# Kernel tuning notes

Hardware: AMD Instinct MI355X
Metric: run time of the kernel (lower is better)

The kernel has to match this reference:

```python
import jax, jax.numpy as jnp
import numpy as np


def setup_inputs() -> dict:
    key = jax.random.key(0)
    kq, kk, kv = jax.random.split(key, 3)
    shape = (2, 16, 2048, 64)  # [B, H, S, D]
    return {
        "q": jax.random.normal(kq, shape, dtype=jnp.float32),
        "k": jax.random.normal(kk, shape, dtype=jnp.float32),
        "v": jax.random.normal(kv, shape, dtype=jnp.float32),
    }


def reference(q, k, v):
    # scores = q @ k^T / sqrt(d_k)  -> [B, H, S, S]
    d_k = k.shape[-1]
    scale = 1.0 / jnp.sqrt(jnp.asarray(d_k, dtype=q.dtype))
    scores = jnp.einsum("bhqd,bhkd->bhqk", q, k) * scale
    seq_len = q.shape[-2]
    # causal mask: position q attends to k <= q
    causal = jnp.tril(jnp.ones((seq_len, seq_len), dtype=bool))
    scores = jnp.where(causal, scores, jnp.asarray(-jnp.inf, dtype=scores.dtype))
    probs = jax.nn.softmax(scores, axis=-1)
    return jnp.einsum("bhqk,bhkd->bhqd", probs, v)
```

## Files before the change

### kernel.cpp

```cpp
#include <hip/hip_runtime.h>
#include <hip/hip_bf16.h>

typedef short bf16x8 __attribute__((ext_vector_type(8)));
typedef short bf16x4 __attribute__((ext_vector_type(4)));
typedef float f32x4  __attribute__((ext_vector_type(4)));
typedef float f32x16 __attribute__((ext_vector_type(16)));

#define D_DIM 64
#define SEQ 2048
#define BHD (SEQ * D_DIM)
#define SCALE_L2E 0.1803368801111204f

__device__ __forceinline__ unsigned short f2bf(float f) {
    unsigned u = __builtin_bit_cast(unsigned, f);
    u += 0x7fffu + ((u >> 16) & 1u);
    return (unsigned short)(u >> 16);
}

__device__ __forceinline__ unsigned swz(unsigned row, unsigned colByte) {
    return (row * 128u + colByte) ^ ((row & 7u) << 4);
}

__device__ __forceinline__ void gl_lds(const unsigned short* g, unsigned char* lds_generic,
                                       unsigned lds_off) {
    __builtin_amdgcn_global_load_lds(
        (const __attribute__((address_space(1))) void*)g,
        (__attribute__((address_space(3))) void*)(lds_generic + lds_off), 16, 0, 0);
}

__device__ __forceinline__ float fexp2(float x) {
    float r; asm("v_exp_f32 %0, %1" : "=v"(r) : "v"(x)); return r;
}
__device__ __forceinline__ unsigned cvtpk(float lo, float hi) {
    unsigned r; asm("v_cvt_pk_bf16_f32 %0, %1, %2" : "=v"(r) : "v"(lo), "v"(hi)); return r;
}

__global__ __launch_bounds__(256) void prep_kernel(const float* __restrict__ K,
                                                   const float* __restrict__ V,
                                                   unsigned short* __restrict__ Kb,
                                                   unsigned short* __restrict__ Vt) {
    __shared__ unsigned short t[64][66];
    const int st = blockIdx.x;
    const int bh = blockIdx.y;
    const int tid = threadIdx.x;
    const size_t base = (size_t)bh * BHD;

    const float* ksrc = K + base + st * 4096;
    unsigned short* kdst = Kb + base + st * 4096;
    #pragma unroll
    for (int j = 0; j < 2; ++j) {
        int e = (j * 256 + tid) * 8;
        float4 a = *(const float4*)(ksrc + e);
        float4 b = *(const float4*)(ksrc + e + 4);
        bf16x8 o;
        o[0] = (short)f2bf(a.x); o[1] = (short)f2bf(a.y);
        o[2] = (short)f2bf(a.z); o[3] = (short)f2bf(a.w);
        o[4] = (short)f2bf(b.x); o[5] = (short)f2bf(b.y);
        o[6] = (short)f2bf(b.z); o[7] = (short)f2bf(b.w);
        *(bf16x8*)(kdst + e) = o;
    }

    const float* vb = V + base + st * 64 * D_DIM;
    #pragma unroll
    for (int j = 0; j < 4; ++j) {
        int n = tid + 256 * j;
        int r = n >> 4;
        int c = (n & 15) << 2;
        float4 v = *(const float4*)(vb + r * D_DIM + c);
        t[r][c + 0] = f2bf(v.x); t[r][c + 1] = f2bf(v.y);
        t[r][c + 2] = f2bf(v.z); t[r][c + 3] = f2bf(v.w);
    }
    __syncthreads();
    #pragma unroll
    for (int j = 0; j < 2; ++j) {
        int m = tid + 256 * j;
        int d = m >> 3;
        int s8 = (m & 7) << 3;
        bf16x8 o;
        #pragma unroll
        for (int e = 0; e < 8; ++e) o[e] = (short)t[s8 + e][d];
        *(bf16x8*)(Vt + base + (size_t)d * SEQ + st * 64 + s8) = o;
    }
}

__global__ __launch_bounds__(512, 4) void attn_fwd(const float* __restrict__ Qp,
                                                   const unsigned short* __restrict__ Kb,
                                                   const unsigned short* __restrict__ Vtb,
                                                   float* __restrict__ Op) {
    __shared__ __align__(16) unsigned char lds[65536];

    int id = blockIdx.y * gridDim.x + blockIdx.x;
    int j  = id >> 3;
    const int bh = (id & 7) * 4 + (j >> 4);
    const int jq = j & 15;
    const int qtile = (j < 32) ? (15 - jq) : jq;

    const int tid  = threadIdx.x;
    const int w    = tid >> 6;
    const int lane = tid & 63;
    const int l31  = lane & 31;
    const int hi2  = lane >> 5;
    const int wsub = w & 3;
    const int par  = w >> 2;

    const int qlo = qtile * 128 + wsub * 32;
    const int t_w = qlo >> 6;
    const int qg  = qlo + l31;
    const int nt  = qtile + 1;

    const size_t base = (size_t)bh * BHD;
    const float* qp = Qp + base;
    const unsigned short* kb = Kb + base;
    const unsigned short* vt = Vtb + base;
    float* op = Op + base;

    const int srow = tid >> 3;
    const int scb  = ((tid & 7) << 4) ^ ((srow & 7) << 4);
    const int kOff = srow * D_DIM + (scb >> 1);
    const int vOff = srow * SEQ + (scb >> 1);
    const unsigned sdst = (unsigned)tid * 16u;

    auto STAGE = [&](int it) {
        unsigned bb = (unsigned)(it & 1) * 32768u;
        const unsigned short* kg = kb + (size_t)(2 * it) * 4096 + kOff;
        const unsigned short* vg = vt + (size_t)(2 * it) * 64 + vOff;
        gl_lds(kg, lds, bb + sdst);
        gl_lds(vg, lds, bb + 8192u + sdst);
        gl_lds(kg + 4096, lds, bb + 16384u + sdst);
        gl_lds(vg + 64, lds, bb + 24576u + sdst);
    };

    const float* qsrc = qp + (size_t)qg * D_DIM + hi2 * 8;
    float4 qraw[8];
    #pragma unroll
    for (int dk = 0; dk < 4; ++dk) {
        qraw[2 * dk]     = *(const float4*)(qsrc + dk * 16);
        qraw[2 * dk + 1] = *(const float4*)(qsrc + dk * 16 + 4);
    }
    STAGE(0);

    bf16x8 qB[4];
    #pragma unroll
    for (int dk = 0; dk < 4; ++dk) {
        float4 a = qraw[2 * dk], b = qraw[2 * dk + 1];
        bf16x8 v;
        v[0] = (short)f2bf(a.x * SCALE_L2E); v[1] = (short)f2bf(a.y * SCALE_L2E);
        v[2] = (short)f2bf(a.z * SCALE_L2E); v[3] = (short)f2bf(a.w * SCALE_L2E);
        v[4] = (short)f2bf(b.x * SCALE_L2E); v[5] = (short)f2bf(b.y * SCALE_L2E);
        v[6] = (short)f2bf(b.z * SCALE_L2E); v[7] = (short)f2bf(b.w * SCALE_L2E);
        qB[dk] = v;
    }

    f32x16 acc0 = {}, acc1 = {};
    float m_r = -3.0e38f, l_r = 0.f;

    #pragma unroll 1
    for (int it = 0; it < nt; ++it) {
        asm volatile("s_waitcnt vmcnt(0)" ::: "memory");
        __builtin_amdgcn_s_barrier();
        __builtin_amdgcn_sched_barrier(0);
        if (it + 1 < nt) STAGE(it + 1);

        const int tile = 2 * it + par;
        if (tile <= t_w) {
            const unsigned kbuf = (unsigned)(it & 1) * 32768u + (unsigned)par * 16384u;
            const unsigned vbuf = kbuf + 8192u;

            f32x16 st0 = {}, st1 = {};
            __builtin_amdgcn_s_setprio(1);
            #pragma unroll
            for (int dk = 0; dk < 4; ++dk) {
                bf16x8 k0 = *(const bf16x8*)&lds[kbuf +
                    swz((unsigned)l31, (unsigned)(dk * 32 + hi2 * 16))];
                bf16x8 k1 = *(const bf16x8*)&lds[kbuf +
                    swz((unsigned)(32 + l31), (unsigned)(dk * 32 + hi2 * 16))];
                st0 = __builtin_amdgcn_mfma_f32_32x32x16_bf16(k0, qB[dk], st0, 0, 0, 0);
                st1 = __builtin_amdgcn_mfma_f32_32x32x16_bf16(k1, qB[dk], st1, 0, 0, 0);
            }
            __builtin_amdgcn_s_setprio(0);

            if (tile == t_w) {
                #pragma unroll
                for (int r = 0; r < 16; ++r) {
                    int kvb = tile * 64 + (r & 3) + 8 * (r >> 2) + 4 * hi2;
                    if (kvb > qg)      st0[r] = -3.0e38f;
                    if (kvb + 32 > qg) st1[r] = -3.0e38f;
                }
            }

            float m8[8];
            #pragma unroll
            for (int r = 0; r < 8; ++r)
                m8[r] = fmaxf(fmaxf(st0[r], st0[r + 8]), fmaxf(st1[r], st1[r + 8]));
            #pragma unroll
            for (int r = 0; r < 4; ++r) m8[r] = fmaxf(m8[r], m8[r + 4]);
            float mx = fmaxf(fmaxf(m8[0], m8[1]), fmaxf(m8[2], m8[3]));
            mx = fmaxf(mx, __shfl_xor(mx, 32));

            float mn;
            if (__all(mx <= m_r + 8.0f)) {
                mn = m_r;
            } else {
                mn = fmaxf(m_r, mx);
                float sc = fexp2(m_r - mn);
                m_r = mn;
                l_r *= sc;
                #pragma unroll
                for (int r = 0; r < 16; ++r) { acc0[r] *= sc; acc1[r] *= sc; }
            }

            #pragma unroll
            for (int r = 0; r < 16; ++r) st0[r] = fexp2(st0[r] - mn);
            #pragma unroll
            for (int r = 0; r < 16; ++r) st1[r] = fexp2(st1[r] - mn);
            float s16[16];
            #pragma unroll
            for (int r = 0; r < 16; ++r) s16[r] = st0[r] + st1[r];
            #pragma unroll
            for (int r = 0; r < 8; ++r) s16[r] += s16[r + 8];
            #pragma unroll
            for (int r = 0; r < 4; ++r) s16[r] += s16[r + 4];
            float rs = (s16[0] + s16[1]) + (s16[2] + s16[3]);
            rs += __shfl_xor(rs, 32);
            l_r += rs;

            bf16x8 pf[4];
            #pragma unroll
            for (int b2 = 0; b2 < 2; ++b2) {
                unsigned W[4][2];
                #pragma unroll
                for (int c = 0; c < 4; ++c) {
                    float v0 = b2 ? st1[4 * c + 0] : st0[4 * c + 0];
                    float v1 = b2 ? st1[4 * c + 1] : st0[4 * c + 1];
                    float v2 = b2 ? st1[4 * c + 2] : st0[4 * c + 2];
                    float v3 = b2 ? st1[4 * c + 3] : st0[4 * c + 3];
                    W[c][0] = cvtpk(v0, v1);
                    W[c][1] = cvtpk(v2, v3);
                }
                #pragma unroll
                for (int m = 0; m < 2; ++m) {
                    unsigned s0 = hi2 ? W[2 * m][0] : W[2 * m + 1][0];
                    unsigned s1 = hi2 ? W[2 * m][1] : W[2 * m + 1][1];
                    unsigned r0 = (unsigned)__shfl_xor((int)s0, 32);
                    unsigned r1 = (unsigned)__shfl_xor((int)s1, 32);
                    int4 fw;
                    fw.x = (int)(hi2 ? r0 : W[2 * m][0]);
                    fw.y = (int)(hi2 ? r1 : W[2 * m][1]);
                    fw.z = (int)(hi2 ? W[2 * m + 1][0] : r0);
                    fw.w = (int)(hi2 ? W[2 * m + 1][1] : r1);
                    pf[b2 * 2 + m] = __builtin_bit_cast(bf16x8, fw);
                }
            }

            __builtin_amdgcn_s_setprio(1);
            #pragma unroll
            for (int mm = 0; mm < 4; ++mm) {
                bf16x8 va0 = *(const bf16x8*)&lds[vbuf +
                    swz((unsigned)l31, (unsigned)(mm * 32 + hi2 * 16))];
                bf16x8 va1 = *(const bf16x8*)&lds[vbuf +
                    swz((unsigned)(32 + l31), (unsigned)(mm * 32 + hi2 * 16))];
                acc0 = __builtin_amdgcn_mfma_f32_32x32x16_bf16(va0, pf[mm], acc0, 0, 0, 0);
                acc1 = __builtin_amdgcn_mfma_f32_32x32x16_bf16(va1, pf[mm], acc1, 0, 0, 0);
            }
            __builtin_amdgcn_s_setprio(0);
        }
    }

    __builtin_amdgcn_s_barrier();
    const unsigned mbase = (unsigned)wsub * (64u * 144u) + (unsigned)lane * 144u;
    if (w >= 4) {
        #pragma unroll
        for (int c = 0; c < 4; ++c) {
            f32x4 q0 = {acc0[4 * c], acc0[4 * c + 1], acc0[4 * c + 2], acc0[4 * c + 3]};
            *(f32x4*)&lds[mbase + c * 16] = q0;
            f32x4 q1 = {acc1[4 * c], acc1[4 * c + 1], acc1[4 * c + 2], acc1[4 * c + 3]};
            *(f32x4*)&lds[mbase + 64 + c * 16] = q1;
        }
        *(float*)&lds[mbase + 128] = m_r;
        *(float*)&lds[mbase + 132] = l_r;
    }
    __builtin_amdgcn_s_barrier();
    if (w < 4) {
        float m2 = *(const float*)&lds[mbase + 128];
        float l2 = *(const float*)&lds[mbase + 132];
        float m  = fmaxf(m_r, m2);
        float a1 = fexp2(m_r - m);
        float a2 = fexp2(m2 - m);
        float l  = a1 * l_r + a2 * l2;
        float inv = 1.f / l;
        #pragma unroll
        for (int c = 0; c < 4; ++c) {
            f32x4 p0 = *(const f32x4*)&lds[mbase + c * 16];
            f32x4 p1 = *(const f32x4*)&lds[mbase + 64 + c * 16];
            float4 o0, o1;
            o0.x = (a1 * acc0[4 * c + 0] + a2 * p0[0]) * inv;
            o0.y = (a1 * acc0[4 * c + 1] + a2 * p0[1]) * inv;
            o0.z = (a1 * acc0[4 * c + 2] + a2 * p0[2]) * inv;
            o0.w = (a1 * acc0[4 * c + 3] + a2 * p0[3]) * inv;
            o1.x = (a1 * acc1[4 * c + 0] + a2 * p1[0]) * inv;
            o1.y = (a1 * acc1[4 * c + 1] + a2 * p1[1]) * inv;
            o1.z = (a1 * acc1[4 * c + 2] + a2 * p1[2]) * inv;
            o1.w = (a1 * acc1[4 * c + 3] + a2 * p1[3]) * inv;
            *(float4*)(op + (size_t)qg * D_DIM + 8 * c + 4 * hi2) = o0;
            *(float4*)(op + (size_t)qg * D_DIM + 32 + 8 * c + 4 * hi2) = o1;
        }
    }
}

__global__ __launch_bounds__(256) void attn_fwd_fb(
    const float* __restrict__ Qp, const float* __restrict__ Kp,
    const float* __restrict__ Vp, float* __restrict__ Op, int S)
{
    __shared__ __align__(16) unsigned char lds_k[64 * 128];
    __shared__ __align__(16) unsigned char lds_vt[64 * 128];
    __shared__ __align__(16) unsigned char lds_p[4 * 16 * 128];

    const int qt = blockIdx.x, bh = blockIdx.y, tid = threadIdx.x;
    const int w = tid >> 6, lane = tid & 63, lo = lane & 15, hi = lane >> 4;
    const size_t base = (size_t)bh * S * D_DIM;
    const float* qp = Qp + base; const float* kp = Kp + base;
    const float* vp = Vp + base; float* op = Op + base;
    const int qw = qt * 64 + w * 16;

    auto swzl = [](unsigned row, unsigned colByte) {
        return (row * 128u + colByte) ^ ((row & 7u) << 4);
    };

    bf16x8 qf[2];
    {
        const float* src = qp + (size_t)(qw + lo) * D_DIM + hi * 8;
        #pragma unroll
        for (int f = 0; f < 2; ++f) {
            float4 a = *(const float4*)(src + f * 32);
            float4 b = *(const float4*)(src + f * 32 + 4);
            bf16x8 v;
            v[0] = (short)f2bf(a.x * 0.125f); v[1] = (short)f2bf(a.y * 0.125f);
            v[2] = (short)f2bf(a.z * 0.125f); v[3] = (short)f2bf(a.w * 0.125f);
            v[4] = (short)f2bf(b.x * 0.125f); v[5] = (short)f2bf(b.y * 0.125f);
            v[6] = (short)f2bf(b.z * 0.125f); v[7] = (short)f2bf(b.w * 0.125f);
            qf[f] = v;
        }
    }
    f32x4 o_acc[4]; float m_r[4], l_r[4];
    #pragma unroll
    for (int r = 0; r < 4; ++r) { m_r[r] = -__builtin_inff(); l_r[r] = 0.f; }
    #pragma unroll
    for (int dt = 0; dt < 4; ++dt) o_acc[dt] = (f32x4){0.f, 0.f, 0.f, 0.f};
    const unsigned pbase = (unsigned)w * 2048u;

    for (int t = 0; t <= qt; ++t) {
        const size_t kv0 = (size_t)t * 64;
        __syncthreads();
        #pragma unroll
        for (int jj = 0; jj < 4; ++jj) {
            int n = tid + 256 * jj;
            int r = n >> 4, c = (n & 15) << 2;
            float4 kk = *(const float4*)(kp + (kv0 + r) * D_DIM + c);
            bf16x4 kbv;
            kbv[0] = (short)f2bf(kk.x); kbv[1] = (short)f2bf(kk.y);
            kbv[2] = (short)f2bf(kk.z); kbv[3] = (short)f2bf(kk.w);
            *(bf16x4*)&lds_k[swzl((unsigned)r, (unsigned)c * 2)] = kbv;
            float4 vv = *(const float4*)(vp + (kv0 + r) * D_DIM + c);
            *(unsigned short*)&lds_vt[swzl((unsigned)(c + 0), (unsigned)r * 2)] = f2bf(vv.x);
            *(unsigned short*)&lds_vt[swzl((unsigned)(c + 1), (unsigned)r * 2)] = f2bf(vv.y);
            *(unsigned short*)&lds_vt[swzl((unsigned)(c + 2), (unsigned)r * 2)] = f2bf(vv.z);
            *(unsigned short*)&lds_vt[swzl((unsigned)(c + 3), (unsigned)r * 2)] = f2bf(vv.w);
        }
        __syncthreads();

        float sc[4][4];
        #pragma unroll
        for (int kc = 0; kc < 4; ++kc) {
            f32x4 s = (f32x4){0.f, 0.f, 0.f, 0.f};
            #pragma unroll
            for (int f = 0; f < 2; ++f) {
                bf16x8 kfv = *(const bf16x8*)&lds_k[swzl((unsigned)(kc * 16 + lo),
                                                         (unsigned)(hi * 16 + f * 64))];
                s = __builtin_amdgcn_mfma_f32_16x16x32_bf16(qf[f], kfv, s, 0, 0, 0);
            }
            #pragma unroll
            for (int r = 0; r < 4; ++r) sc[kc][r] = s[r];
        }
        if (t == qt) {
            #pragma unroll
            for (int kc = 0; kc < 4; ++kc)
                #pragma unroll
                for (int r = 0; r < 4; ++r) {
                    int qg2 = w * 16 + hi * 4 + r, kg = kc * 16 + lo;
                    if (kg > qg2) sc[kc][r] = -__builtin_inff();
                }
        }
        float scale[4];
        #pragma unroll
        for (int r = 0; r < 4; ++r) {
            float mx = fmaxf(fmaxf(sc[0][r], sc[1][r]), fmaxf(sc[2][r], sc[3][r]));
            mx = fmaxf(mx, __shfl_xor(mx, 1)); mx = fmaxf(mx, __shfl_xor(mx, 2));
            mx = fmaxf(mx, __shfl_xor(mx, 4)); mx = fmaxf(mx, __shfl_xor(mx, 8));
            float mn = fmaxf(m_r[r], mx);
            scale[r] = __expf(m_r[r] - mn); m_r[r] = mn;
            float s0 = 0.f;
            #pragma unroll
            for (int kc = 0; kc < 4; ++kc) {
                float pv = __expf(sc[kc][r] - mn); sc[kc][r] = pv; s0 += pv;
            }
            s0 += __shfl_xor(s0, 1); s0 += __shfl_xor(s0, 2);
            s0 += __shfl_xor(s0, 4); s0 += __shfl_xor(s0, 8);
            l_r[r] = l_r[r] * scale[r] + s0;
        }
        #pragma unroll
        for (int r = 0; r < 4; ++r) {
            unsigned qr = (unsigned)(hi * 4 + r);
            #pragma unroll
            for (int kc = 0; kc < 4; ++kc)
                *(unsigned short*)&lds_p[pbase + swzl(qr, (unsigned)((kc * 16 + lo) * 2))] =
                    f2bf(sc[kc][r]);
            #pragma unroll
            for (int dt = 0; dt < 4; ++dt) o_acc[dt][r] *= scale[r];
        }
        bf16x8 pa0 = *(const bf16x8*)&lds_p[pbase + swzl((unsigned)lo, (unsigned)(hi * 16))];
        bf16x8 pa1 = *(const bf16x8*)&lds_p[pbase + swzl((unsigned)lo, (unsigned)(hi * 16 + 64))];
        #pragma unroll
        for (int dt = 0; dt < 4; ++dt) {
            bf16x8 vb0 = *(const bf16x8*)&lds_vt[swzl((unsigned)(dt * 16 + lo), (unsigned)(hi * 16))];
            bf16x8 vb1 = *(const bf16x8*)&lds_vt[swzl((unsigned)(dt * 16 + lo), (unsigned)(hi * 16 + 64))];
            o_acc[dt] = __builtin_amdgcn_mfma_f32_16x16x32_bf16(pa0, vb0, o_acc[dt], 0, 0, 0);
            o_acc[dt] = __builtin_amdgcn_mfma_f32_16x16x32_bf16(pa1, vb1, o_acc[dt], 0, 0, 0);
        }
    }
    const int qrow = qw + hi * 4;
    #pragma unroll
    for (int r = 0; r < 4; ++r) {
        float inv = 1.f / l_r[r];
        #pragma unroll
        for (int dt = 0; dt < 4; ++dt)
            op[(size_t)(qrow + r) * D_DIM + dt * 16 + lo] = o_acc[dt][r] * inv;
    }
}

extern "C" void kernel_launch(void* const* d_in, const int* in_sizes, int n_in,
                              void* d_out, int out_size, void* d_ws, size_t ws_size,
                              hipStream_t stream) {
    const float* q = (const float*)d_in[0];
    const float* k = (const float*)d_in[1];
    const float* v = (const float*)d_in[2];
    float* o = (float*)d_out;

    const size_t nelem = (size_t)32 * BHD;
    const size_t need = 2 * nelem * sizeof(unsigned short);

    if (ws_size >= need) {
        unsigned short* kbf = (unsigned short*)d_ws;
        unsigned short* vtb = kbf + nelem;
        prep_kernel<<<dim3(32, 32), 256, 0, stream>>>(k, v, kbf, vtb);
        attn_fwd<<<dim3(16, 32), 512, 0, stream>>>(q, kbf, vtb, o);
    } else {
        attn_fwd_fb<<<dim3(32, 32), 256, 0, stream>>>(q, k, v, o, SEQ);
    }
}
```

Before: 49.74 us.

## Split KV range four ways across 16 waves per attention block

Rewrites the main attention kernel to use 1024-thread blocks (16 waves), with four wave groups each taking a quarter of the KV tiles for the same 128-row query tile, instead of two. The four partial softmax states are merged through LDS at the end. The block order also changes to a simple longest-first schedule (descending query tile, bh innermost). Shorter per-block loops give more parallelism, but 128KB of LDS per block limits occupancy to one block per CU, and the four-way merge costs extra LDS traffic.

```diff
diff --git a/kernel.cpp b/kernel.cpp
--- a/kernel.cpp
+++ b/kernel.cpp
@@ -16,18 +16,15 @@
     u += 0x7fffu + ((u >> 16) & 1u);
     return (unsigned short)(u >> 16);
 }
-
 __device__ __forceinline__ unsigned swz(unsigned row, unsigned colByte) {
     return (row * 128u + colByte) ^ ((row & 7u) << 4);
 }
-
 __device__ __forceinline__ void gl_lds(const unsigned short* g, unsigned char* lds_generic,
                                        unsigned lds_off) {
     __builtin_amdgcn_global_load_lds(
         (const __attribute__((address_space(1))) void*)g,
         (__attribute__((address_space(3))) void*)(lds_generic + lds_off), 16, 0, 0);
 }
-
 __device__ __forceinline__ float fexp2(float x) {
     float r; asm("v_exp_f32 %0, %1" : "=v"(r) : "v"(x)); return r;
 }
@@ -83,30 +80,28 @@
     }
 }
 
-__global__ __launch_bounds__(512, 4) void attn_fwd(const float* __restrict__ Qp,
-                                                   const unsigned short* __restrict__ Kb,
-                                                   const unsigned short* __restrict__ Vtb,
-                                                   float* __restrict__ Op) {
-    __shared__ __align__(16) unsigned char lds[65536];
-
-    int id = blockIdx.y * gridDim.x + blockIdx.x;
-    int j  = id >> 3;
-    const int bh = (id & 7) * 4 + (j >> 4);
-    const int jq = j & 15;
-    const int qtile = (j < 32) ? (15 - jq) : jq;
+__global__ __launch_bounds__(1024, 4) void attn_fwd16(const float* __restrict__ Qp,
+                                                      const unsigned short* __restrict__ Kb,
+                                                      const unsigned short* __restrict__ Vtb,
+                                                      float* __restrict__ Op) {
+    __shared__ __align__(16) unsigned char lds[131072];
+
+    const int idx = blockIdx.x;
+    const int qt  = 15 - (idx >> 5);
+    const int bh  = idx & 31;
 
     const int tid  = threadIdx.x;
     const int w    = tid >> 6;
     const int lane = tid & 63;
     const int l31  = lane & 31;
     const int hi2  = lane >> 5;
-    const int wsub = w & 3;
-    const int par  = w >> 2;
-
-    const int qlo = qtile * 128 + wsub * 32;
-    const int t_w = qlo >> 6;
+    const int rg   = w & 3;
+    const int p    = w >> 2;
+
+    const int qlo = qt * 128 + rg * 32;
+    const int t_w = 2 * qt + (rg >> 1);
     const int qg  = qlo + l31;
-    const int nt  = qtile + 1;
+    const int nt  = (2 * qt + 5) >> 2;
 
     const size_t base = (size_t)bh * BHD;
     const float* qp = Qp + base;
@@ -114,20 +109,23 @@
     const unsigned short* vt = Vtb + base;
     float* op = Op + base;
 
-    const int srow = tid >> 3;
-    const int scb  = ((tid & 7) << 4) ^ ((srow & 7) << 4);
-    const int kOff = srow * D_DIM + (scb >> 1);
-    const int vOff = srow * SEQ + (scb >> 1);
-    const unsigned sdst = (unsigned)tid * 16u;
+    const int half = tid >> 9;
+    const int q9   = tid & 511;
+    const int Lb   = q9 * 16;
+    const int srow = Lb >> 7;
+    const int scb  = (Lb & 127) ^ ((srow & 7) << 4);
+    const int gOff = half ? (srow * SEQ + (scb >> 1)) : (srow * D_DIM + (scb >> 1));
+    const unsigned dOff = (unsigned)(half * 8192 + q9 * 16);
 
     auto STAGE = [&](int it) {
-        unsigned bb = (unsigned)(it & 1) * 32768u;
-        const unsigned short* kg = kb + (size_t)(2 * it) * 4096 + kOff;
-        const unsigned short* vg = vt + (size_t)(2 * it) * 64 + vOff;
-        gl_lds(kg, lds, bb + sdst);
-        gl_lds(vg, lds, bb + 8192u + sdst);
-        gl_lds(kg + 4096, lds, bb + 16384u + sdst);
-        gl_lds(vg + 64, lds, bb + 24576u + sdst);
+        unsigned bb = (unsigned)(it & 1) * 65536u;
+        #pragma unroll
+        for (int s = 0; s < 4; ++s) {
+            int t4 = it * 4 + s;
+            const unsigned short* g = half ? (vt + (size_t)t4 * 64 + gOff)
+                                           : (kb + (size_t)t4 * 4096 + gOff);
+            gl_lds(g, lds, bb + (unsigned)s * 16384u + dOff);
+        }
     };
 
     const float* qsrc = qp + (size_t)qg * D_DIM + hi2 * 8;
@@ -161,9 +159,9 @@
         __builtin_amdgcn_sched_barrier(0);
         if (it + 1 < nt) STAGE(it + 1);
 
-        const int tile = 2 * it + par;
+        const int tile = it * 4 + p;
         if (tile <= t_w) {
-            const unsigned kbuf = (unsigned)(it & 1) * 32768u + (unsigned)par * 16384u;
+            const unsigned kbuf = (unsigned)(it & 1) * 65536u + (unsigned)p * 16384u;
             const unsigned vbuf = kbuf + 8192u;
 
             f32x16 st0 = {}, st1 = {};
@@ -266,41 +264,54 @@
         }
     }
 
-    __builtin_amdgcn_s_barrier();
-    const unsigned mbase = (unsigned)wsub * (64u * 144u) + (unsigned)lane * 144u;
-    if (w >= 4) {
+    __syncthreads();
+    const unsigned mb = (unsigned)((p - 1) * 4 + rg) * (64u * 144u) + (unsigned)lane * 144u;
+    if (p > 0) {
         #pragma unroll
         for (int c = 0; c < 4; ++c) {
-            f32x4 q0 = {acc0[4 * c], acc0[4 * c + 1], acc0[4 * c + 2], acc0[4 * c + 3]};
-            *(f32x4*)&lds[mbase + c * 16] = q0;
-            f32x4 q1 = {acc1[4 * c], acc1[4 * c + 1], acc1[4 * c + 2], acc1[4 * c + 3]};
-            *(f32x4*)&lds[mbase + 64 + c * 16] = q1;
-        }
-        *(float*)&lds[mbase + 128] = m_r;
-        *(float*)&lds[mbase + 132] = l_r;
-    }
-    __builtin_amdgcn_s_barrier();
-    if (w < 4) {
-        float m2 = *(const float*)&lds[mbase + 128];
-        float l2 = *(const float*)&lds[mbase + 132];
-        float m  = fmaxf(m_r, m2);
-        float a1 = fexp2(m_r - m);
-        float a2 = fexp2(m2 - m);
-        float l  = a1 * l_r + a2 * l2;
+            f32x4 a4 = {acc0[4 * c], acc0[4 * c + 1], acc0[4 * c + 2], acc0[4 * c + 3]};
+            *(f32x4*)&lds[mb + c * 16] = a4;
+            f32x4 b4 = {acc1[4 * c], acc1[4 * c + 1], acc1[4 * c + 2], acc1[4 * c + 3]};
+            *(f32x4*)&lds[mb + 64 + c * 16] = b4;
+        }
+        float2 ml; ml.x = m_r; ml.y = l_r;
+        *(float2*)&lds[mb + 128] = ml;
+    }
+    __syncthreads();
+    if (p == 0) {
+        unsigned pb[3];
+        float m4[3], l4[3];
+        #pragma unroll
+        for (int i = 0; i < 3; ++i) {
+            pb[i] = (unsigned)(i * 4 + rg) * (64u * 144u) + (unsigned)lane * 144u;
+            float2 ml = *(const float2*)&lds[pb[i] + 128];
+            m4[i] = ml.x; l4[i] = ml.y;
+        }
+        float m = fmaxf(fmaxf(m_r, m4[0]), fmaxf(m4[1], m4[2]));
+        float a0 = fexp2(m_r - m);
+        float ai[3];
+        float l = a0 * l_r;
+        #pragma unroll
+        for (int i = 0; i < 3; ++i) { ai[i] = fexp2(m4[i] - m); l += ai[i] * l4[i]; }
         float inv = 1.f / l;
         #pragma unroll
         for (int c = 0; c < 4; ++c) {
-            f32x4 p0 = *(const f32x4*)&lds[mbase + c * 16];
-            f32x4 p1 = *(const f32x4*)&lds[mbase + 64 + c * 16];
             float4 o0, o1;
-            o0.x = (a1 * acc0[4 * c + 0] + a2 * p0[0]) * inv;
-            o0.y = (a1 * acc0[4 * c + 1] + a2 * p0[1]) * inv;
-            o0.z = (a1 * acc0[4 * c + 2] + a2 * p0[2]) * inv;
-            o0.w = (a1 * acc0[4 * c + 3] + a2 * p0[3]) * inv;
-            o1.x = (a1 * acc1[4 * c + 0] + a2 * p1[0]) * inv;
-            o1.y = (a1 * acc1[4 * c + 1] + a2 * p1[1]) * inv;
-            o1.z = (a1 * acc1[4 * c + 2] + a2 * p1[2]) * inv;
-            o1.w = (a1 * acc1[4 * c + 3] + a2 * p1[3]) * inv;
+            o0.x = a0 * acc0[4 * c + 0]; o0.y = a0 * acc0[4 * c + 1];
+            o0.z = a0 * acc0[4 * c + 2]; o0.w = a0 * acc0[4 * c + 3];
+            o1.x = a0 * acc1[4 * c + 0]; o1.y = a0 * acc1[4 * c + 1];
+            o1.z = a0 * acc1[4 * c + 2]; o1.w = a0 * acc1[4 * c + 3];
+            #pragma unroll
+            for (int i = 0; i < 3; ++i) {
+                f32x4 p0 = *(const f32x4*)&lds[pb[i] + c * 16];
+                f32x4 p1 = *(const f32x4*)&lds[pb[i] + 64 + c * 16];
+                o0.x += ai[i] * p0[0]; o0.y += ai[i] * p0[1];
+                o0.z += ai[i] * p0[2]; o0.w += ai[i] * p0[3];
+                o1.x += ai[i] * p1[0]; o1.y += ai[i] * p1[1];
+                o1.z += ai[i] * p1[2]; o1.w += ai[i] * p1[3];
+            }
+            o0.x *= inv; o0.y *= inv; o0.z *= inv; o0.w *= inv;
+            o1.x *= inv; o1.y *= inv; o1.z *= inv; o1.w *= inv;
             *(float4*)(op + (size_t)qg * D_DIM + 8 * c + 4 * hi2) = o0;
             *(float4*)(op + (size_t)qg * D_DIM + 32 + 8 * c + 4 * hi2) = o1;
         }
@@ -452,7 +463,7 @@
         unsigned short* kbf = (unsigned short*)d_ws;
         unsigned short* vtb = kbf + nelem;
         prep_kernel<<<dim3(32, 32), 256, 0, stream>>>(k, v, kbf, vtb);
-        attn_fwd<<<dim3(16, 32), 512, 0, stream>>>(q, kbf, vtb, o);
+        attn_fwd16<<<512, 1024, 0, stream>>>(q, kbf, vtb, o);
     } else {
         attn_fwd_fb<<<dim3(32, 32), 256, 0, stream>>>(q, k, v, o, SEQ);
     }
```

Measured after the change: 52.50 us. 5.6% more time.
